# Kernel optimization log

Hardware: AMD Instinct MI355X
Metric: run time of the kernel (lower is better)

Reference implementation:

```python
import jax, jax.numpy as jnp
import numpy as np

HIDDEN = 1024
HEADS = 16
HEAD_DIM = HIDDEN // HEADS
BATCH = 1
SEQ = 4096
SCALE = 1.0 / np.sqrt(HEAD_DIM)


def setup_inputs() -> dict:
    key = jax.random.key(0)
    ks = jax.random.split(key, 5)
    s = 0.02
    return {
        "hidden_states": jax.random.normal(ks[0], (BATCH, SEQ, HIDDEN), jnp.float32),
        "qkv_w": jax.random.normal(ks[1], (3 * HIDDEN, HIDDEN), jnp.float32) * s,
        "qkv_b": jax.random.normal(ks[2], (3 * HIDDEN,), jnp.float32) * s,
        "out_w": jax.random.normal(ks[3], (HIDDEN, HIDDEN), jnp.float32) * s,
        "out_b": jax.random.normal(ks[4], (HIDDEN,), jnp.float32) * s,
    }


def reference(hidden_states, qkv_w, qkv_b, out_w, out_b):
    B, S, H = hidden_states.shape
    # fused QKV projection (torch Linear: x @ W^T + b)
    qkv = hidden_states @ qkv_w.T + qkv_b              # [B, S, 3H]
    qkv = qkv.reshape(B, S, 3, HEADS, HEAD_DIM)
    qkv = jnp.transpose(qkv, (2, 0, 3, 1, 4))          # [3, B, nh, S, hd]
    q, k, v = qkv[0] * SCALE, qkv[1], qkv[2]
    # ring attention over all KV chunks == full softmax attention
    scores = jnp.einsum('bhqd,bhkd->bhqk', q, k)       # [B, nh, S, S]
    probs = jax.nn.softmax(scores, axis=-1)
    ctx = jnp.einsum('bhqk,bhkd->bhqd', probs, v)      # [B, nh, S, hd]
    ctx = jnp.transpose(ctx, (0, 2, 1, 3)).reshape(B, S, H)
    return ctx @ out_w.T + out_b
```

## Files before the change

kernel.cpp:

```cpp
#include <hip/hip_runtime.h>

#define SEQ 4096
#define HID 1024
#define NHEADS 16
#define HDIM 64
#define QK_SCALE 0.1803368801111204f

typedef float  f32x4 __attribute__((ext_vector_type(4)));
typedef int    i32x4 __attribute__((ext_vector_type(4)));
typedef int    i32x2 __attribute__((ext_vector_type(2)));
typedef __bf16 bf16x8 __attribute__((ext_vector_type(8)));
typedef unsigned short u16;
typedef unsigned int   u32;

static __device__ __forceinline__ u16 f2bf(float f) {
  u32 u = __builtin_bit_cast(u32, f);
  return (u16)((u + 0x7FFFu + ((u >> 16) & 1u)) >> 16);
}
static __device__ __forceinline__ int cvtpk(float lo, float hi) {
  int r;
  asm("v_cvt_pk_bf16_f32 %0, %1, %2" : "=v"(r) : "v"(lo), "v"(hi));
  return r;
}
static __device__ __forceinline__ f32x4 exp2v(f32x4 x) {
  f32x4 o;
  o.x = __builtin_amdgcn_exp2f(x.x);
  o.y = __builtin_amdgcn_exp2f(x.y);
  o.z = __builtin_amdgcn_exp2f(x.z);
  o.w = __builtin_amdgcn_exp2f(x.w);
  return o;
}
static __device__ __forceinline__ float sum4(f32x4 x) {
  return (x.x + x.y) + (x.z + x.w);
}
static __device__ __forceinline__ f32x4 mfma16(i32x4 a, i32x4 b, f32x4 c) {
  return __builtin_amdgcn_mfma_f32_16x16x32_bf16(
      __builtin_bit_cast(bf16x8, a), __builtin_bit_cast(bf16x8, b), c, 0, 0, 0);
}

#define GLD(gsrc, lds_dst)                                        \
  __builtin_amdgcn_global_load_lds(                               \
      (const __attribute__((address_space(1))) void*)(gsrc),      \
      (__attribute__((address_space(3))) void*)(lds_dst), 16, 0, 0)

__global__ __launch_bounds__(256) void cvt_kernel(
    const float* __restrict__ X, const float* __restrict__ Wq,
    const float* __restrict__ Wo, u16* __restrict__ Xb,
    u16* __restrict__ Wqb, u16* __restrict__ Wob) {
  const int u = blockIdx.x * 256 + threadIdx.x;
  const float* src; u16* dst; int local;
  if (u < 524288)       { src = X;  dst = Xb;  local = u; }
  else if (u < 917504)  { src = Wq; dst = Wqb; local = u - 524288; }
  else                  { src = Wo; dst = Wob; local = u - 917504; }
  const int row = local >> 7, gu = local & 127;
  const int w = gu & 7, blk = gu >> 3;
  const int ks = w >> 2, q2 = w & 3;
  const float* s = src + (size_t)row * 1024 + blk * 64 + ks * 32 + q2 * 4;
  float4 x0 = *(const float4*)s;
  float4 x1 = *(const float4*)(s + 16);
  i32x4 o = {cvtpk(x0.x, x0.y), cvtpk(x0.z, x0.w),
             cvtpk(x1.x, x1.y), cvtpk(x1.z, x1.w)};
  *(i32x4*)(dst + (size_t)row * 1024 + blk * 64 + w * 8) = o;
}

static __device__ __forceinline__ void gemm_tile(
    const u16* __restrict__ A, const u16* __restrict__ B,
    int mb, int nb, u16 (*LA)[128][64], u16 (*LB)[128][64],
    f32x4 acc[4][4]) {
  const int t = threadIdx.x, lane = t & 63, wv = t >> 6;
  const int g = lane >> 4, r = lane & 15;
  const int wr = wv >> 1, wc = wv & 1;
  const int lr = lane >> 3, sl = lane & 7;

  const u16* pa = A + (size_t)(mb + wv * 32 + lr) * 1024 + ((sl ^ lr) << 3);
  const u16* pb = B + (size_t)(nb + wv * 32 + lr) * 1024 + ((sl ^ lr) << 3);

  const u16* afp[4][2];
  const u16* bfp[4][2];
#pragma unroll
  for (int i = 0; i < 4; ++i)
#pragma unroll
    for (int ks = 0; ks < 2; ++ks) {
      const int sw = r & 7;
      afp[i][ks] = &LA[0][wr * 64 + i * 16 + r][(((ks * 4 + g) ^ sw) << 3)];
      bfp[i][ks] = &LB[0][wc * 64 + i * 16 + r][(((ks * 4 + g) ^ sw) << 3)];
    }
#pragma unroll
  for (int i = 0; i < 4; ++i)
#pragma unroll
    for (int j = 0; j < 4; ++j) acc[i][j] = (f32x4)0.0f;

#pragma unroll
  for (int j = 0; j < 4; ++j) {
    GLD(pa + j * 8 * 1024, &LA[0][wv * 32 + j * 8][0]);
    GLD(pb + j * 8 * 1024, &LB[0][wv * 32 + j * 8][0]);
  }
  pa += 64; pb += 64;
  __syncthreads();

#define GEMM_STEP(BU, PRE)                                                  \
  {                                                                         \
    if (PRE) {                                                              \
      _Pragma("unroll")                                                     \
      for (int j = 0; j < 4; ++j) {                                         \
        GLD(pa + j * 8 * 1024, &LA[(BU) ^ 1][wv * 32 + j * 8][0]);          \
        GLD(pb + j * 8 * 1024, &LB[(BU) ^ 1][wv * 32 + j * 8][0]);          \
      }                                                                     \
      pa += 64; pb += 64;                                                   \
    }                                                                       \
    i32x4 af[4][2], bf[4][2];                                               \
    _Pragma("unroll")                                                       \
    for (int i = 0; i < 4; ++i)                                             \
      _Pragma("unroll")                                                     \
      for (int ks = 0; ks < 2; ++ks) {                                      \
        af[i][ks] = *(const i32x4*)(afp[i][ks] + (BU) * 8192);              \
        bf[i][ks] = *(const i32x4*)(bfp[i][ks] + (BU) * 8192);              \
      }                                                                     \
    __builtin_amdgcn_s_setprio(1);                                          \
    _Pragma("unroll")                                                       \
    for (int ks = 0; ks < 2; ++ks)                                          \
      _Pragma("unroll")                                                     \
      for (int i = 0; i < 4; ++i)                                           \
        _Pragma("unroll")                                                   \
        for (int j = 0; j < 4; ++j)                                         \
          acc[i][j] = mfma16(af[i][ks], bf[j][ks], acc[i][j]);              \
    __builtin_amdgcn_s_setprio(0);                                          \
    __syncthreads();                                                        \
  }

  for (int kk = 0; kk < 8; ++kk) {
    GEMM_STEP(0, true)
    GEMM_STEP(1, (kk < 7))
  }
#undef GEMM_STEP
}

__global__ __launch_bounds__(256) void qkv_kernel(
    const u16* __restrict__ A, const u16* __restrict__ Bw,
    const float* __restrict__ BI, u16* __restrict__ qws,
    u16* __restrict__ kws, u16* __restrict__ vws) {
  __shared__ u16 LA[2][128][64];
  __shared__ u16 LB[2][128][64];
  const int t = threadIdx.x, lane = t & 63, wv = t >> 6;
  const int g = lane >> 4, r = lane & 15;
  const int wr = wv >> 1, wc = wv & 1;
  const int mb = blockIdx.x * 128, nb = blockIdx.y * 128;

  f32x4 acc[4][4];
  gemm_tile(A, Bw, mb, nb, LA, LB, acc);

#pragma unroll
  for (int ni = 0; ni < 4; ni++) {
    const int n = nb + wc * 64 + ni * 16 + r;
    const float bias = BI[n];
    const int which = n >> 10;
    const int h = (n >> 6) & 15;
    const int d = n & 63;
    u16* dst = (which == 0) ? qws : (which == 1) ? kws : vws;
    const float sc = (which == 0) ? QK_SCALE : 1.0f;
    const int dq = (which == 2)
        ? d
        : ((d & 32) | (((d >> 2) & 3) << 3) | (((d >> 4) & 1) << 2) | (d & 3));
#pragma unroll
    for (int mi = 0; mi < 4; mi++) {
      const int m0 = mb + wr * 64 + mi * 16 + g * 4;
#pragma unroll
      for (int e = 0; e < 4; e += 2) {
        float v0 = (acc[mi][ni][e] + bias) * sc;
        float v1 = (acc[mi][ni][e + 1] + bias) * sc;
        int w = cvtpk(v0, v1);
        dst[((size_t)h * SEQ + m0 + e) * HDIM + dq] = (u16)w;
        dst[((size_t)h * SEQ + m0 + e + 1) * HDIM + dq] = (u16)(w >> 16);
      }
    }
  }
}

__global__ __launch_bounds__(256, 2) void attn_kernel(
    const u16* __restrict__ qws, const u16* __restrict__ kws,
    const u16* __restrict__ vws, u16* __restrict__ ctx) {
  __shared__ u16 Kl[2][64][64];
  __shared__ u16 Vl[2][16][256];
  const int t = threadIdx.x;
  const int lane = t & 63, wv = t >> 6;
  const int g = lane >> 4, r = lane & 15;

  const int fb = blockIdx.x;
  const int swz = (fb & 7) * 64 + (fb >> 3);
  const int h = swz >> 5;
  const int qb = (swz & 31) * 128 + wv * 32;

  i32x4 qf[2][2];
#pragma unroll
  for (int qt = 0; qt < 2; qt++)
#pragma unroll
    for (int db = 0; db < 2; db++)
      qf[qt][db] = *(const i32x4*)(qws +
          ((size_t)(h * SEQ + qb + qt * 16 + r) * HDIM + db * 32 + g * 8));

  f32x4 acc[2][4];
  f32x4 l4[2];
  const f32x4 zero4 = (f32x4)0.0f;
#pragma unroll
  for (int qt = 0; qt < 2; qt++) {
    l4[qt] = (f32x4)0.0f;
#pragma unroll
    for (int dc = 0; dc < 4; dc++) acc[qt][dc] = (f32x4)0.0f;
  }

  const u16* kh_base = kws + (size_t)h * SEQ * HDIM;
  const u16* vh_base = vws + (size_t)h * SEQ * HDIM;

  const u16* kgA = kh_base + (size_t)(16 * wv + (lane >> 3)) * HDIM +
                   (((lane & 7) ^ ((lane >> 3) & 7)) << 3);
  const u16* kgB = kgA + 8 * HDIM;
  const u16* vgA = vh_base +
                   (size_t)(wv * 16 + ((lane & 31) >> 1)) * HDIM +
                   (((((lane >> 5) << 1) | (lane & 1))) << 3);
  const u16* vgB = vgA + 32;

  const u16* kfp0[4];
  const u16* kfp1[4];
#pragma unroll
  for (int kt = 0; kt < 4; ++kt) {
    const int R = kt * 16 + r;
    const int sw = R & 7;
    kfp0[kt] = &Kl[0][R][(g ^ sw) << 3];
    kfp1[kt] = &Kl[0][R][((4 + g) ^ sw) << 3];
  }
  const u32 vbase = (u32)(size_t)(&Vl[0][0][0]) + (u32)lane * 8;

  GLD(kgA, &Kl[0][wv * 16][0]);
  GLD(kgB, &Kl[0][wv * 16 + 8][0]);
  GLD(vgA, &Vl[0][wv * 4][0]);
  GLD(vgB, &Vl[0][wv * 4 + 2][0]);
  kgA += 4096; kgB += 4096; vgA += 4096; vgB += 4096;
  __syncthreads();

#define ATTN_STEP(B, PRE)                                                   \
  {                                                                         \
    if (PRE) {                                                              \
      GLD(kgA, &Kl[(B) ^ 1][wv * 16][0]);                                   \
      GLD(kgB, &Kl[(B) ^ 1][wv * 16 + 8][0]);                               \
      GLD(vgA, &Vl[(B) ^ 1][wv * 4][0]);                                    \
      GLD(vgB, &Vl[(B) ^ 1][wv * 4 + 2][0]);                                \
      kgA += 4096; kgB += 4096; vgA += 4096; vgB += 4096;                   \
    }                                                                       \
    f32x4 st[2][4];                                                         \
    __builtin_amdgcn_s_setprio(1);                                          \
    _Pragma("unroll")                                                       \
    for (int kt = 0; kt < 4; ++kt) {                                        \
      i32x4 kf0 = *(const i32x4*)(kfp0[kt] + (B) * 4096);                   \
      i32x4 kf1 = *(const i32x4*)(kfp1[kt] + (B) * 4096);                   \
      st[0][kt] = mfma16(kf0, qf[0][0], zero4);                             \
      st[0][kt] = mfma16(kf1, qf[0][1], st[0][kt]);                         \
      st[1][kt] = mfma16(kf0, qf[1][0], zero4);                             \
      st[1][kt] = mfma16(kf1, qf[1][1], st[1][kt]);                         \
    }                                                                       \
    __builtin_amdgcn_s_setprio(0);                                          \
                          \
    i32x4 pf[2][2];                                                         \
    _Pragma("unroll")                                                       \
    for (int qt = 0; qt < 2; ++qt) {                                        \
      f32x4 p0 = exp2v(st[qt][0]);                                          \
      f32x4 p1 = exp2v(st[qt][1]);                                          \
      f32x4 p2 = exp2v(st[qt][2]);                                          \
      f32x4 p3 = exp2v(st[qt][3]);                                          \
      l4[qt] += p0; l4[qt] += p1; l4[qt] += p2; l4[qt] += p3;               \
      pf[qt][0] = (i32x4){cvtpk(p0.x, p0.y), cvtpk(p0.z, p0.w),             \
                          cvtpk(p1.x, p1.y), cvtpk(p1.z, p1.w)};            \
      pf[qt][1] = (i32x4){cvtpk(p2.x, p2.y), cvtpk(p2.z, p2.w),             \
                          cvtpk(p3.x, p3.y), cvtpk(p3.z, p3.w)};            \
    }                                                                       \
    const u32 vb = vbase + (B) * 8192;                                      \
    __builtin_amdgcn_s_setprio(1);                                          \
    _Pragma("unroll")                                                       \
    for (int dc = 0; dc < 4; ++dc) {                                        \
      i32x2 t0, t1, t2, t3;                                                 \
      asm volatile(                                                         \
          "ds_read_b64_tr_b16 %0, %4 offset:0\n\t"                          \
          "ds_read_b64_tr_b16 %1, %4 offset:2048\n\t"                       \
          "ds_read_b64_tr_b16 %2, %4 offset:4096\n\t"                       \
          "ds_read_b64_tr_b16 %3, %4 offset:6144"                           \
          : "=&v"(t0), "=&v"(t1), "=&v"(t2), "=&v"(t3)                      \
          : "v"(vb + dc * 512));                                            \
      asm volatile("s_waitcnt lgkmcnt(0)" ::: "memory");                    \
      __builtin_amdgcn_sched_barrier(0);                                    \
      i32x4 vf0 = {t0.x, t0.y, t1.x, t1.y};                                 \
      i32x4 vf1 = {t2.x, t2.y, t3.x, t3.y};                                 \
      acc[0][dc] = mfma16(pf[0][0], vf0, acc[0][dc]);                       \
      acc[0][dc] = mfma16(pf[0][1], vf1, acc[0][dc]);                       \
      acc[1][dc] = mfma16(pf[1][0], vf0, acc[1][dc]);                       \
      acc[1][dc] = mfma16(pf[1][1], vf1, acc[1][dc]);                       \
    }                                                                       \
    __builtin_amdgcn_s_setprio(0);                                          \
    __syncthreads();                                                        \
  }

  for (int cc = 0; cc < 32; ++cc) {
    ATTN_STEP(0, true)
    ATTN_STEP(1, (cc < 31))
  }
#undef ATTN_STEP

#pragma unroll
  for (int qt = 0; qt < 2; ++qt) {
    float lsum = sum4(l4[qt]);
    lsum += __shfl_xor(lsum, 16);
    lsum += __shfl_xor(lsum, 32);
#pragma unroll
    for (int rr = 0; rr < 4; ++rr) {
      const float lr_ = __shfl(lsum, 4 * g + rr);
      const float inv = 1.0f / lr_;
      const int s_ = qb + qt * 16 + 4 * g + rr;
#pragma unroll
      for (int dc = 0; dc < 4; ++dc) {
        const int shuf = ((dc >> 1) << 5) | ((r >> 2) << 3) | ((dc & 1) << 2) | (r & 3);
        ctx[(size_t)s_ * HID + h * HDIM + shuf] = f2bf(acc[qt][dc][rr] * inv);
      }
    }
  }
}

__global__ __launch_bounds__(256) void out_kernel(
    const u16* __restrict__ A, const u16* __restrict__ Bw,
    const float* __restrict__ BI, float* __restrict__ out) {
  __shared__ u16 LA[2][128][64];
  __shared__ u16 LB[2][128][64];
  const int t = threadIdx.x, lane = t & 63, wv = t >> 6;
  const int g = lane >> 4, r = lane & 15;
  const int wr = wv >> 1, wc = wv & 1;
  const int mb = blockIdx.x * 128, nb = blockIdx.y * 128;

  f32x4 acc[4][4];
  gemm_tile(A, Bw, mb, nb, LA, LB, acc);

#pragma unroll
  for (int ni = 0; ni < 4; ni++) {
    const int n = nb + wc * 64 + ni * 16 + r;
    const float bias = BI[n];
#pragma unroll
    for (int mi = 0; mi < 4; mi++) {
      const int m0 = mb + wr * 64 + mi * 16 + g * 4;
#pragma unroll
      for (int e = 0; e < 4; e++)
        out[(size_t)(m0 + e) * HID + n] = acc[mi][ni][e] + bias;
    }
  }
}

extern "C" void kernel_launch(void* const* d_in, const int* in_sizes, int n_in,
                              void* d_out, int out_size, void* d_ws, size_t ws_size,
                              hipStream_t stream) {
  const float* X    = (const float*)d_in[0];
  const float* Wqkv = (const float*)d_in[1];
  const float* Bqkv = (const float*)d_in[2];
  const float* Wout = (const float*)d_in[3];
  const float* Bout = (const float*)d_in[4];
  float* out = (float*)d_out;

  const size_t per = (size_t)NHEADS * SEQ * HDIM;
  u16* qws = (u16*)d_ws;
  u16* kws = qws + per;
  u16* vws = kws + per;
  u16* xbctx = vws + per;
  u16* wqb = xbctx + per;
  u16* wob = wqb + (size_t)3072 * 1024;

  cvt_kernel<<<4096, 256, 0, stream>>>(X, Wqkv, Wout, xbctx, wqb, wob);
  qkv_kernel<<<dim3(32, 24), 256, 0, stream>>>(xbctx, wqb, Bqkv, qws, kws, vws);
  attn_kernel<<<dim3(512), 256, 0, stream>>>(qws, kws, vws, xbctx);
  out_kernel<<<dim3(32, 8), 256, 0, stream>>>(xbctx, wob, Bout, out);
}
```

Measured before the change: 141.0 us.

## Store V transposed from QKV projection and read it with plain LDS loads

The QKV epilogue now writes V in a transposed, per-head [d][seq] layout with a permuted sequence order, using packed 32-bit stores. The attention kernel stages V^T tiles through swizzled shared memory the same way it stages K. It then reads PV operands with ordinary 128-bit LDS loads, which removes the ds_read_b64_tr_b16 transpose reads and their explicit lgkmcnt waits and scheduling barriers. The cost is scattered 4-byte global stores for V in the projection kernel and strided (row = seq length) global loads for V tiles.

```diff
diff --git a/kernel.cpp b/kernel.cpp
--- a/kernel.cpp
+++ b/kernel.cpp
@@ -138,7 +138,7 @@
 __global__ __launch_bounds__(256) void qkv_kernel(
     const u16* __restrict__ A, const u16* __restrict__ Bw,
     const float* __restrict__ BI, u16* __restrict__ qws,
-    u16* __restrict__ kws, u16* __restrict__ vws) {
+    u16* __restrict__ kws, u16* __restrict__ vtws) {
   __shared__ u16 LA[2][128][64];
   __shared__ u16 LB[2][128][64];
   const int t = threadIdx.x, lane = t & 63, wv = t >> 6;
@@ -156,21 +156,36 @@
     const int which = n >> 10;
     const int h = (n >> 6) & 15;
     const int d = n & 63;
-    u16* dst = (which == 0) ? qws : (which == 1) ? kws : vws;
-    const float sc = (which == 0) ? QK_SCALE : 1.0f;
-    const int dq = (which == 2)
-        ? d
-        : ((d & 32) | (((d >> 2) & 3) << 3) | (((d >> 4) & 1) << 2) | (d & 3));
-#pragma unroll
-    for (int mi = 0; mi < 4; mi++) {
-      const int m0 = mb + wr * 64 + mi * 16 + g * 4;
-#pragma unroll
-      for (int e = 0; e < 4; e += 2) {
-        float v0 = (acc[mi][ni][e] + bias) * sc;
-        float v1 = (acc[mi][ni][e + 1] + bias) * sc;
-        int w = cvtpk(v0, v1);
-        dst[((size_t)h * SEQ + m0 + e) * HDIM + dq] = (u16)w;
-        dst[((size_t)h * SEQ + m0 + e + 1) * HDIM + dq] = (u16)(w >> 16);
+    if (which == 2) {
+      u16* base = vtws + (((size_t)(h * 64 + d)) << 12) + mb + wr * 64;
+#pragma unroll
+      for (int mi = 0; mi < 4; mi++) {
+#pragma unroll
+        for (int e = 0; e < 4; e += 2) {
+          float v0 = acc[mi][ni][e] + bias;
+          float v1 = acc[mi][ni][e + 1] + bias;
+          const int s6 = mi * 16 + g * 4 + e;
+          const int pos = (s6 & 32) | (((s6 >> 2) & 3) << 3) |
+                          (((s6 >> 4) & 1) << 2) | (s6 & 3);
+          *(u32*)(base + pos) = (u32)cvtpk(v0, v1);
+        }
+      }
+    } else {
+      u16* dst = which ? kws : qws;
+      const float sc = which ? 1.0f : QK_SCALE;
+      const int dq = ((d & 32) | (((d >> 2) & 3) << 3) |
+                      (((d >> 4) & 1) << 2) | (d & 3));
+#pragma unroll
+      for (int mi = 0; mi < 4; mi++) {
+        const int m0 = mb + wr * 64 + mi * 16 + g * 4;
+#pragma unroll
+        for (int e = 0; e < 4; e += 2) {
+          float v0 = (acc[mi][ni][e] + bias) * sc;
+          float v1 = (acc[mi][ni][e + 1] + bias) * sc;
+          int w = cvtpk(v0, v1);
+          dst[((size_t)h * SEQ + m0 + e) * HDIM + dq] = (u16)w;
+          dst[((size_t)h * SEQ + m0 + e + 1) * HDIM + dq] = (u16)(w >> 16);
+        }
       }
     }
   }
@@ -178,9 +193,9 @@
 
 __global__ __launch_bounds__(256, 2) void attn_kernel(
     const u16* __restrict__ qws, const u16* __restrict__ kws,
-    const u16* __restrict__ vws, u16* __restrict__ ctx) {
+    const u16* __restrict__ vtws, u16* __restrict__ ctx) {
   __shared__ u16 Kl[2][64][64];
-  __shared__ u16 Vl[2][16][256];
+  __shared__ u16 Vtl[2][64][64];
   const int t = threadIdx.x;
   const int lane = t & 63, wv = t >> 6;
   const int g = lane >> 4, r = lane & 15;
@@ -209,32 +224,35 @@
   }
 
   const u16* kh_base = kws + (size_t)h * SEQ * HDIM;
-  const u16* vh_base = vws + (size_t)h * SEQ * HDIM;
-
-  const u16* kgA = kh_base + (size_t)(16 * wv + (lane >> 3)) * HDIM +
-                   (((lane & 7) ^ ((lane >> 3) & 7)) << 3);
+  const u16* vt_base = vtws + ((size_t)h << 18);
+
+  const int lr8 = lane >> 3, sl = lane & 7;
+  const u16* kgA = kh_base + (size_t)(16 * wv + lr8) * HDIM +
+                   ((sl ^ (lr8 & 7)) << 3);
   const u16* kgB = kgA + 8 * HDIM;
-  const u16* vgA = vh_base +
-                   (size_t)(wv * 16 + ((lane & 31) >> 1)) * HDIM +
-                   (((((lane >> 5) << 1) | (lane & 1))) << 3);
-  const u16* vgB = vgA + 32;
+  const u16* vtgA = vt_base + (size_t)(16 * wv + lr8) * SEQ +
+                    ((sl ^ (lr8 & 7)) << 3);
+  const u16* vtgB = vtgA + (size_t)8 * SEQ;
 
   const u16* kfp0[4];
   const u16* kfp1[4];
-#pragma unroll
-  for (int kt = 0; kt < 4; ++kt) {
-    const int R = kt * 16 + r;
+  const u16* vfp0[4];
+  const u16* vfp1[4];
+#pragma unroll
+  for (int i = 0; i < 4; ++i) {
+    const int R = i * 16 + r;
     const int sw = R & 7;
-    kfp0[kt] = &Kl[0][R][(g ^ sw) << 3];
-    kfp1[kt] = &Kl[0][R][((4 + g) ^ sw) << 3];
-  }
-  const u32 vbase = (u32)(size_t)(&Vl[0][0][0]) + (u32)lane * 8;
+    kfp0[i] = &Kl[0][R][(g ^ sw) << 3];
+    kfp1[i] = &Kl[0][R][((4 + g) ^ sw) << 3];
+    vfp0[i] = &Vtl[0][R][(g ^ sw) << 3];
+    vfp1[i] = &Vtl[0][R][((4 + g) ^ sw) << 3];
+  }
 
   GLD(kgA, &Kl[0][wv * 16][0]);
   GLD(kgB, &Kl[0][wv * 16 + 8][0]);
-  GLD(vgA, &Vl[0][wv * 4][0]);
-  GLD(vgB, &Vl[0][wv * 4 + 2][0]);
-  kgA += 4096; kgB += 4096; vgA += 4096; vgB += 4096;
+  GLD(vtgA, &Vtl[0][wv * 16][0]);
+  GLD(vtgB, &Vtl[0][wv * 16 + 8][0]);
+  kgA += 4096; kgB += 4096; vtgA += 64; vtgB += 64;
   __syncthreads();
 
 #define ATTN_STEP(B, PRE)                                                   \
@@ -242,9 +260,9 @@
     if (PRE) {                                                              \
       GLD(kgA, &Kl[(B) ^ 1][wv * 16][0]);                                   \
       GLD(kgB, &Kl[(B) ^ 1][wv * 16 + 8][0]);                               \
-      GLD(vgA, &Vl[(B) ^ 1][wv * 4][0]);                                    \
-      GLD(vgB, &Vl[(B) ^ 1][wv * 4 + 2][0]);                                \
-      kgA += 4096; kgB += 4096; vgA += 4096; vgB += 4096;                   \
+      GLD(vtgA, &Vtl[(B) ^ 1][wv * 16][0]);                                 \
+      GLD(vtgB, &Vtl[(B) ^ 1][wv * 16 + 8][0]);                             \
+      kgA += 4096; kgB += 4096; vtgA += 64; vtgB += 64;                     \
     }                                                                       \
     f32x4 st[2][4];                                                         \
     __builtin_amdgcn_s_setprio(1);                                          \
@@ -272,22 +290,12 @@
       pf[qt][1] = (i32x4){cvtpk(p2.x, p2.y), cvtpk(p2.z, p2.w),             \
                           cvtpk(p3.x, p3.y), cvtpk(p3.z, p3.w)};            \
     }                                                                       \
-    const u32 vb = vbase + (B) * 8192;                                      \
+     \
     __builtin_amdgcn_s_setprio(1);                                          \
     _Pragma("unroll")                                                       \
     for (int dc = 0; dc < 4; ++dc) {                                        \
-      i32x2 t0, t1, t2, t3;                                                 \
-      asm volatile(                                                         \
-          "ds_read_b64_tr_b16 %0, %4 offset:0\n\t"                          \
-          "ds_read_b64_tr_b16 %1, %4 offset:2048\n\t"                       \
-          "ds_read_b64_tr_b16 %2, %4 offset:4096\n\t"                       \
-          "ds_read_b64_tr_b16 %3, %4 offset:6144"                           \
-          : "=&v"(t0), "=&v"(t1), "=&v"(t2), "=&v"(t3)                      \
-          : "v"(vb + dc * 512));                                            \
-      asm volatile("s_waitcnt lgkmcnt(0)" ::: "memory");                    \
-      __builtin_amdgcn_sched_barrier(0);                                    \
-      i32x4 vf0 = {t0.x, t0.y, t1.x, t1.y};                                 \
-      i32x4 vf1 = {t2.x, t2.y, t3.x, t3.y};                                 \
+      i32x4 vf0 = *(const i32x4*)(vfp0[dc] + (B) * 4096);                   \
+      i32x4 vf1 = *(const i32x4*)(vfp1[dc] + (B) * 4096);                   \
       acc[0][dc] = mfma16(pf[0][0], vf0, acc[0][dc]);                       \
       acc[0][dc] = mfma16(pf[0][1], vf1, acc[0][dc]);                       \
       acc[1][dc] = mfma16(pf[1][0], vf0, acc[1][dc]);                       \
@@ -362,13 +370,13 @@
   const size_t per = (size_t)NHEADS * SEQ * HDIM;
   u16* qws = (u16*)d_ws;
   u16* kws = qws + per;
-  u16* vws = kws + per;
-  u16* xbctx = vws + per;
+  u16* vtws = kws + per;
+  u16* xbctx = vtws + per;
   u16* wqb = xbctx + per;
   u16* wob = wqb + (size_t)3072 * 1024;
 
   cvt_kernel<<<4096, 256, 0, stream>>>(X, Wqkv, Wout, xbctx, wqb, wob);
-  qkv_kernel<<<dim3(32, 24), 256, 0, stream>>>(xbctx, wqb, Bqkv, qws, kws, vws);
-  attn_kernel<<<dim3(512), 256, 0, stream>>>(qws, kws, vws, xbctx);
+  qkv_kernel<<<dim3(32, 24), 256, 0, stream>>>(xbctx, wqb, Bqkv, qws, kws, vtws);
+  attn_kernel<<<dim3(512), 256, 0, stream>>>(qws, kws, vtws, xbctx);
   out_kernel<<<dim3(32, 8), 256, 0, stream>>>(xbctx, wob, Bout, out);
 }
```

After: 138.6 us. About the same (-1.7%).
